# Optimization experiments

Hardware: AMD Instinct MI355X
Metric: run time of the kernel (lower is better)

## Reference

```python
import jax, jax.numpy as jnp
import numpy as np

B, S, D, H = 2, 2048, 1024, 16
HD = D // H  # 64


def setup_inputs() -> dict:
    key = jax.random.key(0)
    ks = jax.random.split(key, 6)
    x = jax.random.normal(ks[0], (B, S, D), dtype=jnp.float32)
    # rotary frequencies: theta = 10000^{-2i/hd}, angles = pos * theta
    inv_freq = 1.0 / (10000.0 ** (jnp.arange(0, HD, 2, dtype=jnp.float32) / HD))  # [HD/2]
    angles = jnp.arange(S, dtype=jnp.float32)[:, None] * inv_freq[None, :]  # [S, HD/2]
    freqs_cos = jnp.cos(angles)
    freqs_sin = jnp.sin(angles)
    scale = 0.02
    w_qkv = jax.random.normal(ks[1], (3 * D, D), dtype=jnp.float32) * scale
    b_qkv = jnp.zeros((3 * D,), dtype=jnp.float32)
    w_dense = jax.random.normal(ks[2], (D, D), dtype=jnp.float32) * scale
    b_dense = jnp.zeros((D,), dtype=jnp.float32)
    return {"x": x, "w_qkv": w_qkv, "b_qkv": b_qkv, "w_dense": w_dense,
            "b_dense": b_dense, "freqs_cos": freqs_cos, "freqs_sin": freqs_sin}


def _apply_rope(t, cos, sin):
    # t: [B, S, H, HD]; cos/sin: [S, HD/2] broadcast as [1, S, 1, HD/2]
    tr = t.reshape(t.shape[:-1] + (HD // 2, 2))
    x0, x1 = tr[..., 0], tr[..., 1]
    c = cos[None, :, None, :]
    s = sin[None, :, None, :]
    o0 = x0 * c - x1 * s  # real part of complex multiply
    o1 = x0 * s + x1 * c  # imag part
    return jnp.stack([o0, o1], axis=-1).reshape(t.shape)


def reference(x, w_qkv, b_qkv, w_dense, b_dense, freqs_cos, freqs_sin):
    b, s, d = x.shape
    qkv = x @ w_qkv.T + b_qkv              # [B, S, 3D]
    qkv = qkv.reshape(b, s, 3, H, HD)
    q, k, v = qkv[:, :, 0], qkv[:, :, 1], qkv[:, :, 2]  # [B, S, H, HD]
    q = _apply_rope(q, freqs_cos, freqs_sin)
    k = _apply_rope(k, freqs_cos, freqs_sin)
    # causal SDPA, scale = 1/sqrt(head_dim)
    q = q.transpose(0, 2, 1, 3)  # [B, H, S, HD]
    k = k.transpose(0, 2, 1, 3)
    v = v.transpose(0, 2, 1, 3)
    scores = jnp.einsum('bhqd,bhkd->bhqk', q, k) / jnp.sqrt(jnp.float32(HD))
    causal = jnp.tril(jnp.ones((s, s), dtype=bool))
    scores = jnp.where(causal[None, None], scores, jnp.finfo(scores.dtype).min)
    attn = jax.nn.softmax(scores, axis=-1)
    ctx = jnp.einsum('bhqk,bhkd->bhqd', attn, v)   # [B, H, S, HD]
    ctx = ctx.transpose(0, 2, 1, 3).reshape(b, s, d)
    return ctx @ w_dense.T + b_dense
```

## Files before the change

### kernel.cpp

```cpp
#include <hip/hip_runtime.h>
#include <stdint.h>

#define Bb 2
#define Ss 2048
#define Dd 1024
#define Hh 16
#define HDd 64

typedef float f32x4 __attribute__((ext_vector_type(4)));
typedef __bf16 bf16x8 __attribute__((ext_vector_type(8)));
typedef __bf16 bf16x2 __attribute__((ext_vector_type(2)));
typedef short s16x8 __attribute__((ext_vector_type(8)));

__device__ inline unsigned short f2bf(float f) {
  unsigned u = __builtin_bit_cast(unsigned, f);
  u += 0x7fffu + ((u >> 16) & 1u);
  return (unsigned short)(u >> 16);
}
__device__ inline float bf2f(unsigned short h) {
  unsigned u = ((unsigned)h) << 16;
  return __builtin_bit_cast(float, u);
}
__device__ inline unsigned pkcvt(float a, float b) {
  bf16x2 v;
  v[0] = (__bf16)a;
  v[1] = (__bf16)b;
  return __builtin_bit_cast(unsigned, v);
}
__device__ inline float ex2(float x) {
#if __has_builtin(__builtin_amdgcn_exp2f)
  return __builtin_amdgcn_exp2f(x);
#else
  float r;
  asm("v_exp_f32 %0, %1\n\ts_nop 1" : "=v"(r) : "v"(x));
  return r;
#endif
}
__device__ inline int swz(int row, int soff) {
  return (row << 6) + ((((soff >> 3) ^ (row & 7)) << 3) | (soff & 7));
}

#define GLDS(dst, src)                                                        \
  __builtin_amdgcn_global_load_lds(                                           \
      (const __attribute__((address_space(1))) void*)(src),                   \
      (__attribute__((address_space(3))) void*)(dst), 16, 0, 0)

__global__ void cast_all(const float* __restrict__ x, const float* __restrict__ wq,
                         const float* __restrict__ wd, unsigned short* __restrict__ dst) {
  int i0 = (blockIdx.x * blockDim.x + threadIdx.x) * 2;
#pragma unroll
  for (int e = 0; e < 2; ++e) {
    int i = i0 + e;
    float4 v;
    if (i < 1048576) v = ((const float4*)x)[i];
    else if (i < 1835008) v = ((const float4*)wq)[i - 1048576];
    else v = ((const float4*)wd)[i - 1835008];
    ushort4 o;
    o.x = f2bf(v.x); o.y = f2bf(v.y); o.z = f2bf(v.z); o.w = f2bf(v.w);
    ((ushort4*)dst)[i] = o;
  }
}

__global__ __launch_bounds__(256, 2) void gemm_qkv(
    const unsigned short* __restrict__ A, const unsigned short* __restrict__ Bw,
    const float* __restrict__ bias, unsigned short* __restrict__ qkvout,
    unsigned short* __restrict__ vtout,
    const float* __restrict__ fc, const float* __restrict__ fs) {
  const int K = 1024, NT = 16;
  __shared__ __align__(16) unsigned short Ah[2][2][128 * 32];
  __shared__ __align__(16) unsigned short Bh[2][2][192 * 32];
  const int tid = threadIdx.x;
  const int w = tid >> 6, l = tid & 63;
  const int lg = l >> 4, lr = l & 15;
  const int wm = w >> 1, wn = w & 1;
  int id = blockIdx.y * gridDim.x + blockIdx.x;
  const int nwg = gridDim.x * gridDim.y;
  id = (id & 7) * (nwg >> 3) + (id >> 3);
  const int bx = id % gridDim.x, by = id / gridDim.x;
  const int mbase = by * 128, nbase = bx * 192;

  const unsigned short* ap[4];
  const unsigned short* bp[6];
#pragma unroll
  for (int i = 0; i < 4; ++i) {
    int c = i * 256 + tid;
    int hf = c >= 512, cw = c & 511;
    int row = cw >> 2, sl = (cw & 3) ^ ((row >> 1) & 3);
    ap[i] = A + (size_t)(mbase + row) * K + hf * 32 + sl * 8;
  }
#pragma unroll
  for (int i = 0; i < 6; ++i) {
    int c = i * 256 + tid;
    int hf = c >= 768, cw = c - hf * 768;
    int row = cw >> 2, sl = (cw & 3) ^ ((row >> 1) & 3);
    bp[i] = Bw + (size_t)(nbase + row) * K + hf * 32 + sl * 8;
  }
#define STAGE(buf, k0)                                                        \
  _Pragma("unroll")                                                           \
  for (int i = 0; i < 4; ++i)                                                 \
    GLDS(&Ah[buf][0][0] + (i * 256 + tid) * 8, ap[i] + (k0));                 \
  _Pragma("unroll")                                                           \
  for (int i = 0; i < 6; ++i)                                                 \
    GLDS(&Bh[buf][0][0] + (i * 256 + tid) * 8, bp[i] + (k0));

  STAGE(0, 0);
  __syncthreads();

  f32x4 acc[4][6] = {};
  for (int t = 0; t < NT; ++t) {
    const int cur = t & 1;
    if (t + 1 < NT) { STAGE(cur ^ 1, (t + 1) * 64); }
#pragma unroll
    for (int h = 0; h < 2; ++h) {
      bf16x8 bfr[6], af[4];
#pragma unroll
      for (int ni = 0; ni < 6; ++ni) {
        int row = wn * 96 + ni * 16 + lr;
        bfr[ni] = *(const bf16x8*)(&Bh[cur][h][row * 32 + ((lg ^ ((row >> 1) & 3)) << 3)]);
      }
#pragma unroll
      for (int j = 0; j < 4; ++j) {
        int row = wm * 64 + j * 16 + lr;
        af[j] = *(const bf16x8*)(&Ah[cur][h][row * 32 + ((lg ^ ((row >> 1) & 3)) << 3)]);
      }
      __builtin_amdgcn_s_setprio(1);
#pragma unroll
      for (int j = 0; j < 4; ++j)
#pragma unroll
        for (int ni = 0; ni < 6; ++ni)
          acc[j][ni] = __builtin_amdgcn_mfma_f32_16x16x32_bf16(
              af[j], bfr[ni], acc[j][ni], 0, 0, 0);
      __builtin_amdgcn_s_setprio(0);
    }
    __syncthreads();
  }
#undef STAGE

#pragma unroll
  for (int mi = 0; mi < 4; ++mi)
#pragma unroll
    for (int ni = 0; ni < 6; ++ni) {
      int col = nbase + wn * 96 + ni * 16 + lr;
      float bi = bias[col];
      int row0 = mbase + wm * 64 + mi * 16 + lg * 4;
      float o4[4];
#pragma unroll
      for (int r = 0; r < 4; ++r) o4[r] = acc[mi][ni][r] + bi;
      int sect = col >> 10;
      int d = col & 63;
      int srow0 = row0 & 2047;
      if (sect < 2) {
        int p = d >> 1;
#pragma unroll
        for (int r = 0; r < 4; ++r) {
          float vp = __shfl_xor(o4[r], 1);
          float c = fc[(srow0 + r) * 32 + p];
          float s = fs[(srow0 + r) * 32 + p];
          float o = (d & 1) ? (vp * s + o4[r] * c) : (o4[r] * c - vp * s);
          qkvout[(size_t)(row0 + r) * 3072 + col] = f2bf(o);
        }
      } else {
        int bh = (row0 >> 11) * 16 + ((col >> 6) & 15);
        uint2 o;
        o.x = pkcvt(o4[0], o4[1]);
        o.y = pkcvt(o4[2], o4[3]);
        *(uint2*)&vtout[((size_t)(bh * 64 + d)) * 2048 + srow0] = o;
      }
    }
}

__global__ __launch_bounds__(256, 2) void gemm_out(
    const unsigned short* __restrict__ A, const unsigned short* __restrict__ Bw,
    const float* __restrict__ bias, float* __restrict__ Cout) {
  const int M = 4096, N = 1024, K = 1024;
  __shared__ __align__(16) unsigned short As[64 * 32];
  __shared__ __align__(16) unsigned short Bs[128 * 32];
  const int tid = threadIdx.x;
  const int w = tid >> 6, l = tid & 63;
  const int lg = l >> 4, lr = l & 15;
  const int wm = w >> 1, wn = w & 1;
  int id = blockIdx.y * gridDim.x + blockIdx.x;
  const int nwg = gridDim.x * gridDim.y;
  id = (id & 7) * (nwg >> 3) + (id >> 3);
  const int bx = id % gridDim.x, by = id / gridDim.x;
  const int mbase = by * 64, nbase = bx * 128;

  const unsigned short *as0, *bs0, *bs1;
  {
    int r_ = tid >> 2, s_ = (tid & 3) ^ ((r_ >> 1) & 3);
    as0 = A + (size_t)(mbase + r_) * K + s_ * 8;
    bs0 = Bw + (size_t)(nbase + r_) * K + s_ * 8;
    int r2 = 64 + r_, s2 = (tid & 3) ^ ((r2 >> 1) & 3);
    bs1 = Bw + (size_t)(nbase + r2) * K + s2 * 8;
  }

  f32x4 acc[2][4] = {};
  for (int k0 = 0; k0 < K; k0 += 32) {
    GLDS(As + tid * 8, as0 + k0);
    GLDS(Bs + tid * 8, bs0 + k0);
    GLDS(Bs + (256 + tid) * 8, bs1 + k0);
    __syncthreads();
    bf16x8 af[2], bfr[4];
#pragma unroll
    for (int mi = 0; mi < 2; ++mi) {
      int row = wm * 32 + mi * 16 + lr;
      af[mi] = *(const bf16x8*)(As + row * 32 + ((lg ^ ((row >> 1) & 3)) << 3));
    }
#pragma unroll
    for (int ni = 0; ni < 4; ++ni) {
      int row = wn * 64 + ni * 16 + lr;
      bfr[ni] = *(const bf16x8*)(Bs + row * 32 + ((lg ^ ((row >> 1) & 3)) << 3));
    }
    __builtin_amdgcn_s_setprio(1);
#pragma unroll
    for (int mi = 0; mi < 2; ++mi)
#pragma unroll
      for (int ni = 0; ni < 4; ++ni)
        acc[mi][ni] = __builtin_amdgcn_mfma_f32_16x16x32_bf16(
            af[mi], bfr[ni], acc[mi][ni], 0, 0, 0);
    __builtin_amdgcn_s_setprio(0);
    __syncthreads();
  }

#pragma unroll
  for (int mi = 0; mi < 2; ++mi) {
#pragma unroll
    for (int ni = 0; ni < 4; ++ni) {
      int col = nbase + wn * 64 + ni * 16 + lr;
      float bi = bias[col];
#pragma unroll
      for (int r = 0; r < 4; ++r) {
        int row = mbase + wm * 32 + mi * 16 + lg * 4 + r;
        Cout[(size_t)row * N + col] = acc[mi][ni][r] + bi;
      }
    }
  }
}

__global__ __launch_bounds__(256, 3) void attn(
    const unsigned short* __restrict__ qkv, const unsigned short* __restrict__ vt,
    unsigned short* __restrict__ ctx) {
  __shared__ __align__(16) unsigned short Ks[2][64 * 64];
  __shared__ __align__(16) unsigned short Vs[2][64 * 64];
  __shared__ __align__(16) unsigned short Ps[4][32 * 64];
  int did = blockIdx.x;
  int x = did & 7, rest = did >> 3;
  int bh = x * 4 + (rest & 3);
  int qi = 31 - (rest >> 2);
  int b = bh >> 4, h = bh & 15;
  int qbase = qi * 64;
  int tid = threadIdx.x;
  int w = tid >> 6, l = tid & 63;
  int lg = l >> 4, lr = l & 15;
  int wq = w & 1, wk = w >> 1;
  int qw = wq * 32;

  bf16x8 qb[2][2];
#pragma unroll
  for (int mi = 0; mi < 2; ++mi)
#pragma unroll
    for (int kc = 0; kc < 2; ++kc) {
      s16x8 qr = *(const s16x8*)(qkv +
          (size_t)(b * Ss + qbase + qw + mi * 16 + lr) * 3072 + h * 64 + kc * 32 + lg * 8);
      bf16x8 qs;
#pragma unroll
      for (int e = 0; e < 8; ++e)
        qs[e] = (__bf16)(bf2f((unsigned short)qr[e]) * 0.18033688f);
      qb[mi][kc] = qs;
    }

  int c1 = tid, c2 = 256 + tid;
  int r1 = c1 >> 3, s1 = ((c1 & 7) ^ (r1 & 7)) * 8;
  int r2 = c2 >> 3, s2 = ((c2 & 7) ^ (r2 & 7)) * 8;
  const unsigned short* kg1 = qkv + ((size_t)(b * Ss) + r1) * 3072 + 1024 + h * 64 + s1;
  const unsigned short* kg2 = qkv + ((size_t)(b * Ss) + r2) * 3072 + 1024 + h * 64 + s2;
  const unsigned short* vg1 = vt + ((size_t)bh * 64 + r1) * 2048 + s1;
  const unsigned short* vg2 = vt + ((size_t)bh * 64 + r2) * 2048 + s2;
#define STAGEKV(kt)                                                           \
  {                                                                           \
    int tt_ = (kt) & 1;                                                       \
    GLDS(&Ks[tt_][0] + c1 * 8, kg1 + (size_t)(kt) * 64 * 3072);               \
    GLDS(&Ks[tt_][0] + c2 * 8, kg2 + (size_t)(kt) * 64 * 3072);               \
    GLDS(&Vs[tt_][0] + c1 * 8, vg1 + (kt) * 64);                              \
    GLDS(&Vs[tt_][0] + c2 * 8, vg2 + (kt) * 64);                              \
  }

  int nkt = qi + 1;
  int nsup = (nkt + 1) >> 1;

  STAGEKV(0);
  if (1 < nkt) STAGEKV(1);
  __syncthreads();

  f32x4 acc[4][2] = {};
  float mrow[2] = {-1e30f, -1e30f}, lsum[2] = {0.f, 0.f};

  for (int j = 0; j < nsup; ++j) {
    int kt = 2 * j + wk;
    if (kt < nkt) {
      f32x4 st[4][2] = {};
      __builtin_amdgcn_s_setprio(1);
#pragma unroll
      for (int kc = 0; kc < 2; ++kc) {
#pragma unroll
        for (int ni = 0; ni < 4; ++ni) {
          bf16x8 ka = *(const bf16x8*)&Ks[wk][swz(ni * 16 + lr, kc * 32 + lg * 8)];
#pragma unroll
          for (int mi = 0; mi < 2; ++mi)
            st[ni][mi] = __builtin_amdgcn_mfma_f32_16x16x32_bf16(
                ka, qb[mi][kc], st[ni][mi], 0, 0, 0);
        }
      }
      __builtin_amdgcn_s_setprio(0);

      float tm[2] = {-1e30f, -1e30f};
      if (kt == qi) {
#pragma unroll
        for (int mi = 0; mi < 2; ++mi) {
          int rq = qw + mi * 16 + lr;
#pragma unroll
          for (int ni = 0; ni < 4; ++ni)
#pragma unroll
            for (int r4 = 0; r4 < 4; ++r4) {
              float s = st[ni][mi][r4];
              if (ni * 16 + lg * 4 + r4 > rq) s = -1e30f;
              st[ni][mi][r4] = s;
              tm[mi] = fmaxf(tm[mi], s);
            }
        }
      } else {
#pragma unroll
        for (int mi = 0; mi < 2; ++mi)
#pragma unroll
          for (int ni = 0; ni < 4; ++ni)
#pragma unroll
            for (int r4 = 0; r4 < 4; ++r4) tm[mi] = fmaxf(tm[mi], st[ni][mi][r4]);
      }
      bool ok = (tm[0] <= mrow[0] + 8.0f) && (tm[1] <= mrow[1] + 8.0f);
      if (!__all(ok)) {
#pragma unroll
        for (int mi = 0; mi < 2; ++mi) {
          float t = fmaxf(tm[mi], __shfl_xor(tm[mi], 16));
          t = fmaxf(t, __shfl_xor(t, 32));
          float mnew = fmaxf(mrow[mi], t);
          float alpha = ex2(mrow[mi] - mnew);
          lsum[mi] *= alpha;
#pragma unroll
          for (int nd = 0; nd < 4; ++nd)
#pragma unroll
            for (int r4 = 0; r4 < 4; ++r4) acc[nd][mi][r4] *= alpha;
          mrow[mi] = mnew;
        }
      }
#pragma unroll
      for (int mi = 0; mi < 2; ++mi) {
        float sum = 0.f;
#pragma unroll
        for (int ni = 0; ni < 4; ++ni)
#pragma unroll
          for (int r4 = 0; r4 < 4; ++r4) {
            float pe = ex2(st[ni][mi][r4] - mrow[mi]);
            st[ni][mi][r4] = pe;
            sum += pe;
          }
        lsum[mi] += sum;
#pragma unroll
        for (int ni = 0; ni < 4; ++ni) {
          uint2 wv;
          wv.x = pkcvt(st[ni][mi][0], st[ni][mi][1]);
          wv.y = pkcvt(st[ni][mi][2], st[ni][mi][3]);
          *(uint2*)&Ps[w][swz(mi * 16 + lr, ni * 16 + lg * 4)] = wv;
        }
      }
      __builtin_amdgcn_s_setprio(1);
#pragma unroll
      for (int kc = 0; kc < 2; ++kc) {
        bf16x8 pbf[2];
#pragma unroll
        for (int mi = 0; mi < 2; ++mi)
          pbf[mi] = *(const bf16x8*)&Ps[w][swz(mi * 16 + lr, kc * 32 + lg * 8)];
#pragma unroll
        for (int nd = 0; nd < 4; ++nd) {
          bf16x8 va = *(const bf16x8*)&Vs[wk][swz(nd * 16 + lr, kc * 32 + lg * 8)];
#pragma unroll
          for (int mi = 0; mi < 2; ++mi)
            acc[nd][mi] = __builtin_amdgcn_mfma_f32_16x16x32_bf16(
                va, pbf[mi], acc[nd][mi], 0, 0, 0);
        }
      }
      __builtin_amdgcn_s_setprio(0);
    }

    if (j + 1 < nsup) {
      __syncthreads();
      int t0 = 2 * (j + 1), t1 = t0 + 1;
      STAGEKV(t0);
      if (t1 < nkt) STAGEKV(t1);
      __syncthreads();
    }
  }
#undef STAGEKV

#pragma unroll
  for (int mi = 0; mi < 2; ++mi) {
    lsum[mi] += __shfl_xor(lsum[mi], 16);
    lsum[mi] += __shfl_xor(lsum[mi], 32);
  }
  __syncthreads();
  float* aS0 = (float*)Ks;
  float* aS1 = (float*)Vs;
  float* mlS = (float*)Ps;
  if (wk == 1) {
    int base = (wq * 64 + l) * 16;
#pragma unroll
    for (int nd = 0; nd < 4; ++nd) {
      *(f32x4*)(aS0 + base + nd * 4) = acc[nd][0];
      *(f32x4*)(aS1 + base + nd * 4) = acc[nd][1];
    }
    int mb = (wq * 64 + l) * 4;
    mlS[mb] = mrow[0]; mlS[mb + 1] = lsum[0];
    mlS[mb + 2] = mrow[1]; mlS[mb + 3] = lsum[1];
  }
  __syncthreads();
  if (wk == 0) {
    int base = (wq * 64 + l) * 16;
    int mb = (wq * 64 + l) * 4;
#pragma unroll
    for (int mi = 0; mi < 2; ++mi) {
      const float* as = (mi ? aS1 : aS0) + base;
      float m1 = mlS[mb + mi * 2], l1 = mlS[mb + mi * 2 + 1];
      float M = fmaxf(mrow[mi], m1);
      float s0 = ex2(mrow[mi] - M), s1 = ex2(m1 - M);
      float inv = 1.0f / (lsum[mi] * s0 + l1 * s1);
      float f0 = s0 * inv, f1 = s1 * inv;
      int qg = qbase + qw + mi * 16 + lr;
#pragma unroll
      for (int nd = 0; nd < 4; ++nd) {
        f32x4 a1 = *(const f32x4*)(as + nd * 4);
        uint2 o;
        o.x = pkcvt(acc[nd][mi][0] * f0 + a1[0] * f1,
                    acc[nd][mi][1] * f0 + a1[1] * f1);
        o.y = pkcvt(acc[nd][mi][2] * f0 + a1[2] * f1,
                    acc[nd][mi][3] * f0 + a1[3] * f1);
        *(uint2*)&ctx[((size_t)(b * Ss) + qg) * 1024 + h * 64 + nd * 16 + lg * 4] = o;
      }
    }
  }
}

extern "C" void kernel_launch(void* const* d_in, const int* in_sizes, int n_in,
                              void* d_out, int out_size, void* d_ws, size_t ws_size,
                              hipStream_t stream) {
  const float* x       = (const float*)d_in[0];
  const float* w_qkv   = (const float*)d_in[1];
  const float* b_qkv   = (const float*)d_in[2];
  const float* w_dense = (const float*)d_in[3];
  const float* b_dense = (const float*)d_in[4];
  const float* fc      = (const float*)d_in[5];
  const float* fs      = (const float*)d_in[6];
  float* out = (float*)d_out;

  char* ws = (char*)d_ws;
  unsigned short* xb    = (unsigned short*)(ws);
  unsigned short* wqkvb = (unsigned short*)(ws + (8ull  << 20));
  unsigned short* wdb   = (unsigned short*)(ws + (14ull << 20));
  unsigned short* qkvb  = (unsigned short*)(ws + (16ull << 20));
  unsigned short* vt    = (unsigned short*)(ws + (40ull << 20));

  cast_all<<<4096, 256, 0, stream>>>(x, w_qkv, w_dense, xb);

  gemm_qkv<<<dim3(16, 32), 256, 0, stream>>>(xb, wqkvb, b_qkv, qkvb, vt, fc, fs);
  attn<<<1024, 256, 0, stream>>>(qkvb, vt, xb );
  gemm_out<<<dim3(8, 64), 256, 0, stream>>>(xb, wdb, b_dense, out);
}
```

Baseline: 109.4 us.

## Single-buffer QKV GEMM LDS to raise occupancy; one float4 per thread in cast

The QKV GEMM drops its double-buffered LDS staging for a single buffer, loading each K-tile and then syncing before compute. This halves shared memory and raises launch bounds to 4 blocks per CU, trading explicit prefetch overlap for more resident waves to hide latency. The cast kernel now converts one float4 per thread over twice as many blocks. The risk is that losing the prefetch exposes global load latency inside every K iteration, and the larger occupancy target may squeeze registers for the 4x6 accumulator tile.

```diff
diff --git a/kernel.cpp b/kernel.cpp
--- a/kernel.cpp
+++ b/kernel.cpp
@@ -47,28 +47,24 @@
 
 __global__ void cast_all(const float* __restrict__ x, const float* __restrict__ wq,
                          const float* __restrict__ wd, unsigned short* __restrict__ dst) {
-  int i0 = (blockIdx.x * blockDim.x + threadIdx.x) * 2;
-#pragma unroll
-  for (int e = 0; e < 2; ++e) {
-    int i = i0 + e;
-    float4 v;
-    if (i < 1048576) v = ((const float4*)x)[i];
-    else if (i < 1835008) v = ((const float4*)wq)[i - 1048576];
-    else v = ((const float4*)wd)[i - 1835008];
-    ushort4 o;
-    o.x = f2bf(v.x); o.y = f2bf(v.y); o.z = f2bf(v.z); o.w = f2bf(v.w);
-    ((ushort4*)dst)[i] = o;
-  }
-}
-
-__global__ __launch_bounds__(256, 2) void gemm_qkv(
+  int i = blockIdx.x * blockDim.x + threadIdx.x;
+  float4 v;
+  if (i < 1048576) v = ((const float4*)x)[i];
+  else if (i < 1835008) v = ((const float4*)wq)[i - 1048576];
+  else v = ((const float4*)wd)[i - 1835008];
+  ushort4 o;
+  o.x = f2bf(v.x); o.y = f2bf(v.y); o.z = f2bf(v.z); o.w = f2bf(v.w);
+  ((ushort4*)dst)[i] = o;
+}
+
+__global__ __launch_bounds__(256, 4) void gemm_qkv(
     const unsigned short* __restrict__ A, const unsigned short* __restrict__ Bw,
     const float* __restrict__ bias, unsigned short* __restrict__ qkvout,
     unsigned short* __restrict__ vtout,
     const float* __restrict__ fc, const float* __restrict__ fs) {
   const int K = 1024, NT = 16;
-  __shared__ __align__(16) unsigned short Ah[2][2][128 * 32];
-  __shared__ __align__(16) unsigned short Bh[2][2][192 * 32];
+  __shared__ __align__(16) unsigned short Ah[2][128 * 32];
+  __shared__ __align__(16) unsigned short Bh[2][192 * 32];
   const int tid = threadIdx.x;
   const int w = tid >> 6, l = tid & 63;
   const int lg = l >> 4, lr = l & 15;
@@ -95,33 +91,29 @@
     int row = cw >> 2, sl = (cw & 3) ^ ((row >> 1) & 3);
     bp[i] = Bw + (size_t)(nbase + row) * K + hf * 32 + sl * 8;
   }
-#define STAGE(buf, k0)                                                        \
-  _Pragma("unroll")                                                           \
-  for (int i = 0; i < 4; ++i)                                                 \
-    GLDS(&Ah[buf][0][0] + (i * 256 + tid) * 8, ap[i] + (k0));                 \
-  _Pragma("unroll")                                                           \
-  for (int i = 0; i < 6; ++i)                                                 \
-    GLDS(&Bh[buf][0][0] + (i * 256 + tid) * 8, bp[i] + (k0));
-
-  STAGE(0, 0);
-  __syncthreads();
 
   f32x4 acc[4][6] = {};
   for (int t = 0; t < NT; ++t) {
-    const int cur = t & 1;
-    if (t + 1 < NT) { STAGE(cur ^ 1, (t + 1) * 64); }
+    const int k0 = t * 64;
+#pragma unroll
+    for (int i = 0; i < 4; ++i)
+      GLDS(&Ah[0][0] + (i * 256 + tid) * 8, ap[i] + k0);
+#pragma unroll
+    for (int i = 0; i < 6; ++i)
+      GLDS(&Bh[0][0] + (i * 256 + tid) * 8, bp[i] + k0);
+    __syncthreads();
 #pragma unroll
     for (int h = 0; h < 2; ++h) {
       bf16x8 bfr[6], af[4];
 #pragma unroll
       for (int ni = 0; ni < 6; ++ni) {
         int row = wn * 96 + ni * 16 + lr;
-        bfr[ni] = *(const bf16x8*)(&Bh[cur][h][row * 32 + ((lg ^ ((row >> 1) & 3)) << 3)]);
+        bfr[ni] = *(const bf16x8*)(&Bh[h][row * 32 + ((lg ^ ((row >> 1) & 3)) << 3)]);
       }
 #pragma unroll
       for (int j = 0; j < 4; ++j) {
         int row = wm * 64 + j * 16 + lr;
-        af[j] = *(const bf16x8*)(&Ah[cur][h][row * 32 + ((lg ^ ((row >> 1) & 3)) << 3)]);
+        af[j] = *(const bf16x8*)(&Ah[h][row * 32 + ((lg ^ ((row >> 1) & 3)) << 3)]);
       }
       __builtin_amdgcn_s_setprio(1);
 #pragma unroll
@@ -134,7 +126,6 @@
     }
     __syncthreads();
   }
-#undef STAGE
 
 #pragma unroll
   for (int mi = 0; mi < 4; ++mi)
@@ -467,7 +458,7 @@
   unsigned short* qkvb  = (unsigned short*)(ws + (16ull << 20));
   unsigned short* vt    = (unsigned short*)(ws + (40ull << 20));
 
-  cast_all<<<4096, 256, 0, stream>>>(x, w_qkv, w_dense, xb);
+  cast_all<<<8192, 256, 0, stream>>>(x, w_qkv, w_dense, xb);
 
   gemm_qkv<<<dim3(16, 32), 256, 0, stream>>>(xb, wqkvb, b_qkv, qkvb, vt, fc, fs);
   attn<<<1024, 256, 0, stream>>>(qkvb, vt, xb );
```

After: 194.2 us. 77.6% more time.
